# Kernel optimization log

Hardware: AMD Instinct MI355X
Metric: run time of the kernel (lower is better)

The kernel has to match this reference:

```python
import jax, jax.numpy as jnp
import numpy as np

SEQ_LEN = 16384
IN_DIM = 2048
STATE_DIM = 2048


def setup_inputs() -> dict:
    key = jax.random.key(0)
    k_xs, k_lam, k_win, k_c, k_d = jax.random.split(key, 5)
    xs = jax.random.normal(k_xs, (SEQ_LEN, IN_DIM), dtype=jnp.float32)
    # diagonal state-transition values in (0, 1) for stability
    lam = jax.random.uniform(k_lam, (STATE_DIM,), dtype=jnp.float32)
    w_in = jax.random.normal(k_win, (STATE_DIM, IN_DIM), dtype=jnp.float32) / np.float32(np.sqrt(IN_DIM))
    c_out = jax.random.normal(k_c, (IN_DIM, STATE_DIM), dtype=jnp.float32) / np.float32(np.sqrt(STATE_DIM))
    d_skip = jax.random.normal(k_d, (IN_DIM,), dtype=jnp.float32)
    return {"xs": xs, "lam": lam, "w_in": w_in, "c_out": c_out, "d_skip": d_skip}


def _ssm_cell(a, b):
    # Faithful replication of BaseSSMLayer.ssm_cell (including its use of
    # matrix_pow_i * matrix_pow_i for the first component, exactly as in source).
    matrix_pow_i, bx_i = a
    matrix_pow_j, bx_j = b
    return (matrix_pow_i * matrix_pow_i, matrix_pow_j * bx_i + bx_j)


def reference(xs, lam, w_in, c_out, d_skip):
    seq_len = xs.shape[0]
    # discretize: broadcast diagonal lambda over the sequence -> [L, N]
    lambda_elements = jnp.broadcast_to(lam, (seq_len, lam.shape[0]))
    # preprocess_inputs: vmap(w_in @ x) == xs @ w_in.T  -> [L, N]
    w_in_xs = jnp.einsum('li,ni->ln', xs, w_in)
    _, hs = jax.lax.associative_scan(_ssm_cell, (lambda_elements, w_in_xs))
    # postprocess: y_t = C h_t + D * x_t  -> [L, in_dim]
    return jnp.einsum('ln,on->lo', hs, c_out) + xs * d_skip
```

## Files before the change

### kernel.cpp

```cpp
#include <hip/hip_runtime.h>

#define SEQ   16384
#define DIM   2048
#define CHUNK 128
#define NCHUNK (SEQ / CHUNK)

typedef __attribute__((ext_vector_type(8))) short  short8;
typedef __attribute__((ext_vector_type(4))) short  short4v;
typedef __attribute__((ext_vector_type(4))) float  floatx4;

static __device__ __forceinline__ float bf2f(short s) {
    return __uint_as_float(((unsigned)(unsigned short)s) << 16);
}
static __device__ __forceinline__ short f2bf(float f) {
    unsigned u = __float_as_uint(f);
    u += 0x7fff + ((u >> 16) & 1);
    return (short)(u >> 16);
}

#define NB_XS (SEQ * DIM / 4 / 256)
#define NB_W  (DIM * DIM / 4 / 256)
__global__ void cast3_kernel(const float* __restrict__ xs,   short* __restrict__ xs_o,
                             const float* __restrict__ w,    short* __restrict__ w_o,
                             const float* __restrict__ c,    short* __restrict__ c_o)
{
    int b = blockIdx.x;
    const float* in; short* out; int i;
    if (b < NB_XS)            { in = xs; out = xs_o; i = b * 256 + threadIdx.x; }
    else if (b < NB_XS + NB_W){ in = w;  out = w_o;  i = (b - NB_XS) * 256 + threadIdx.x; }
    else                      { in = c;  out = c_o;  i = (b - NB_XS - NB_W) * 256 + threadIdx.x; }
    float4 v = ((const float4*)in)[i];
    short4v s;
    s.x = f2bf(v.x); s.y = f2bf(v.y); s.z = f2bf(v.z); s.w = f2bf(v.w);
    ((short4v*)out)[i] = s;
}


#define BAR   __builtin_amdgcn_s_barrier()
#define PRIO1 __builtin_amdgcn_s_setprio(1)
#define PRIO0 __builtin_amdgcn_s_setprio(0)
#define VMC2  asm volatile("s_waitcnt vmcnt(2)" ::: "memory")
#define VMC1  asm volatile("s_waitcnt vmcnt(1)" ::: "memory")
#define VMC0  asm volatile("s_waitcnt vmcnt(0)" ::: "memory")

#define STAGE_A(b, h, t) do { \
    const short* _s = Abase + (size_t)(h) * 128 * K + (size_t)(t) * 64; \
    __builtin_amdgcn_global_load_lds(_s + gOff0, &As[b][h][c0 * 8], 16, 0, 0); \
    __builtin_amdgcn_global_load_lds(_s + gOff1, &As[b][h][c1 * 8], 16, 0, 0); \
} while (0)
#define STAGE_B(b, h, t) do { \
    const short* _s = Bbase + (size_t)(h) * 128 * K + (size_t)(t) * 64; \
    __builtin_amdgcn_global_load_lds(_s + gOff0, &Bs[b][h][c0 * 8], 16, 0, 0); \
    __builtin_amdgcn_global_load_lds(_s + gOff1, &Bs[b][h][c1 * 8], 16, 0, 0); \
} while (0)

#define READ_A8(dst, b, mh) \
    _Pragma("unroll") \
    for (int mi = 0; mi < 4; mi++) { \
        _Pragma("unroll") \
        for (int ks = 0; ks < 2; ks++) \
            dst[mi][ks] = *(const short8*)&As[b][mh][(arow + mi * 16) * 64 + \
                                                     ((((ks << 2) | quad) ^ sx) << 3)]; \
    }
#define READ_B4(dst, b, nh) \
    _Pragma("unroll") \
    for (int ni = 0; ni < 2; ni++) { \
        _Pragma("unroll") \
        for (int ks = 0; ks < 2; ks++) \
            dst[ni][ks] = *(const short8*)&Bs[b][nh][(brow + ni * 16) * 64 + \
                                                     ((((ks << 2) | quad) ^ sx) << 3)]; \
    }
#define MMA(mh, nh, Aset, Bset) \
    _Pragma("unroll") \
    for (int mi = 0; mi < 4; mi++) { \
        _Pragma("unroll") \
        for (int ni = 0; ni < 2; ni++) { \
            acc[mh][nh][mi][ni] = __builtin_amdgcn_mfma_f32_16x16x32_bf16( \
                Aset[mi][0], Bset[ni][0], acc[mh][nh][mi][ni], 0, 0, 0); \
            acc[mh][nh][mi][ni] = __builtin_amdgcn_mfma_f32_16x16x32_bf16( \
                Aset[mi][1], Bset[ni][1], acc[mh][nh][mi][ni], 0, 0, 0); \
        } \
    }

template<int FUSE>
__global__ __launch_bounds__(512, 2)
void gemm_bt(const short* __restrict__ A, const short* __restrict__ B,
             short* __restrict__ Cbf, float* __restrict__ Cf,
             const float* __restrict__ xs, const float* __restrict__ dskip)
{
    constexpr int K  = DIM;
    constexpr int NT = K / 64;

    __shared__ alignas(16) short As[2][2][128 * 64];
    __shared__ alignas(16) short Bs[2][2][128 * 64];

    const int tid = threadIdx.x;
    const int raw  = blockIdx.y * gridDim.x + blockIdx.x;
    const int xcd  = raw & 7;
    const int slot = raw >> 3;
    const int m0   = ((xcd << 3) | (slot >> 3)) * 256;
    const int n0   = (slot & 7) * 256;

    const int lane = tid & 63;
    const int wv   = tid >> 6;
    const int wrow = wv >> 2;
    const int wcol = wv & 3;
    const int l16  = lane & 15;
    const int quad = lane >> 4;
    const int sx   = l16 & 7;
    const int arow = wrow * 64 + l16;
    const int brow = wcol * 32 + l16;

    const int c0 = tid, c1 = tid + 512;
    const int r0 = c0 >> 3, r1 = c1 >> 3;
    const size_t gOff0 = (size_t)r0 * K + (size_t)((((c0 & 7) ^ (r0 & 7))) * 8);
    const size_t gOff1 = (size_t)r1 * K + (size_t)((((c1 & 7) ^ (r1 & 7))) * 8);
    const short* Abase = A + (size_t)m0 * K;
    const short* Bbase = B + (size_t)n0 * K;

    short8  aE[4][2], aO[4][2], bE[2][2], bO[2][2];
    floatx4 acc[2][2][4][2] = {};

    STAGE_A(0, 0, 0); STAGE_B(0, 0, 0); STAGE_B(0, 1, 0);
    STAGE_A(0, 1, 0);
    VMC1;
    BAR;
    READ_A8(aE, 0, 0); READ_B4(bE, 0, 0);

    for (int i = 0; i < NT / 2; ++i) {
        const int t1 = 2 * i + 1;
        const int t2 = (2 * i + 2) & (NT - 1);

        READ_B4(bO, 0, 1);
        STAGE_A(1, 0, t1); STAGE_B(1, 0, t1);
        PRIO1; MMA(0, 0, aE, bE); PRIO0;
        VMC2;
        BAR;
        READ_A8(aO, 0, 1);
        STAGE_B(1, 1, t1); STAGE_A(1, 1, t1);
        PRIO1; MMA(0, 1, aE, bO); PRIO0;
        VMC2;
        BAR;
        PRIO1; MMA(1, 0, aO, bE); PRIO0;
        READ_B4(bE, 1, 0);
        BAR;
        PRIO1; MMA(1, 1, aO, bO); PRIO0;
        READ_A8(aE, 1, 0);
        VMC1;
        BAR;

        READ_B4(bO, 1, 1);
        STAGE_A(0, 0, t2); STAGE_B(0, 0, t2);
        PRIO1; MMA(0, 0, aE, bE); PRIO0;
        VMC2;
        BAR;

        READ_A8(aO, 1, 1);
        STAGE_B(0, 1, t2); STAGE_A(0, 1, t2);
        PRIO1; MMA(0, 1, aE, bO); PRIO0;
        VMC2;
        BAR;

        PRIO1; MMA(1, 0, aO, bE); PRIO0;
        READ_B4(bE, 0, 0);
        BAR;

        PRIO1; MMA(1, 1, aO, bO); PRIO0;
        READ_A8(aE, 0, 0);
        VMC1;
        BAR;
    }
    VMC0;

    if (FUSE == 0) {
        #pragma unroll
        for (int mh = 0; mh < 2; mh++)
        #pragma unroll
        for (int mi = 0; mi < 4; mi++) {
            const int rb = m0 + wrow * 64 + mh * 128 + mi * 16 + quad * 4;
            #pragma unroll
            for (int nh = 0; nh < 2; nh++)
            #pragma unroll
            for (int ni = 0; ni < 2; ni++) {
                const int cc = n0 + wcol * 32 + nh * 128 + ni * 16 + l16;
                #pragma unroll
                for (int r = 0; r < 4; r++)
                    Cbf[(size_t)(rb + r) * DIM + cc] = f2bf(acc[mh][nh][mi][ni][r]);
            }
        }
    } else {
        float dsk[2][2];
        #pragma unroll
        for (int nh = 0; nh < 2; nh++)
        #pragma unroll
        for (int ni = 0; ni < 2; ni++)
            dsk[nh][ni] = dskip[n0 + wcol * 32 + nh * 128 + ni * 16 + l16];
        #pragma unroll
        for (int mh = 0; mh < 2; mh++)
        #pragma unroll
        for (int mi = 0; mi < 4; mi++) {
            const int rb = m0 + wrow * 64 + mh * 128 + mi * 16 + quad * 4;
            #pragma unroll
            for (int nh = 0; nh < 2; nh++)
            #pragma unroll
            for (int ni = 0; ni < 2; ni++) {
                const int cc = n0 + wcol * 32 + nh * 128 + ni * 16 + l16;
                #pragma unroll
                for (int r = 0; r < 4; r++) {
                    size_t idx = (size_t)(rb + r) * DIM + cc;
                    Cf[idx] = acc[mh][nh][mi][ni][r] + xs[idx] * dsk[nh][ni];
                }
            }
        }
    }
}

__global__ void scan_pass1(const short* __restrict__ bx, const float* __restrict__ lam,
                           float* __restrict__ blockLast)
{
    int q     = blockIdx.x * 256 + threadIdx.x;
    int n     = q * 4;
    int chunk = blockIdx.y;
    float4 lm = *(const float4*)&lam[n];
    const uint2* p = (const uint2*)(bx + (size_t)chunk * CHUNK * DIM) + q;
    float h0 = 0.f, h1 = 0.f, h2 = 0.f, h3 = 0.f;
    #pragma unroll 16
    for (int i = 0; i < CHUNK; i++) {
        uint2 v = p[(size_t)i * (DIM / 4)];
        h0 = fmaf(lm.x, h0, bf2f((short)(v.x & 0xffffu)));
        h1 = fmaf(lm.y, h1, bf2f((short)(v.x >> 16)));
        h2 = fmaf(lm.z, h2, bf2f((short)(v.y & 0xffffu)));
        h3 = fmaf(lm.w, h3, bf2f((short)(v.y >> 16)));
    }
    float4 o; o.x = h0; o.y = h1; o.z = h2; o.w = h3;
    *(float4*)&blockLast[(size_t)chunk * DIM + n] = o;
}

__global__ void scan_pass2(float* __restrict__ blockLast, const float* __restrict__ lam)
{
    int n = blockIdx.x * 256 + threadIdx.x;
    float lm = lam[n];
    float p = lm;
    #pragma unroll
    for (int i = 0; i < 7; i++) p = p * p;
    float carry = 0.f;
    #pragma unroll 4
    for (int c = 0; c < NCHUNK; c++) {
        float t = blockLast[(size_t)c * DIM + n];
        blockLast[(size_t)c * DIM + n] = carry;
        carry = fmaf(p, carry, t);
    }
}

__global__ void scan_pass3(short* __restrict__ bxh, const float* __restrict__ lam,
                           const float* __restrict__ carry)
{
    int q     = blockIdx.x * 256 + threadIdx.x;
    int n     = q * 4;
    int chunk = blockIdx.y;
    float4 lm = *(const float4*)&lam[n];
    float4 cv = *(const float4*)&carry[(size_t)chunk * DIM + n];
    float h0 = cv.x, h1 = cv.y, h2 = cv.z, h3 = cv.w;
    uint2* p = (uint2*)(bxh + (size_t)chunk * CHUNK * DIM) + q;
    #pragma unroll 16
    for (int i = 0; i < CHUNK; i++) {
        uint2 v = p[(size_t)i * (DIM / 4)];
        h0 = fmaf(lm.x, h0, bf2f((short)(v.x & 0xffffu)));
        h1 = fmaf(lm.y, h1, bf2f((short)(v.x >> 16)));
        h2 = fmaf(lm.z, h2, bf2f((short)(v.y & 0xffffu)));
        h3 = fmaf(lm.w, h3, bf2f((short)(v.y >> 16)));
        uint2 o;
        o.x = (unsigned)(unsigned short)f2bf(h0) | ((unsigned)(unsigned short)f2bf(h1) << 16);
        o.y = (unsigned)(unsigned short)f2bf(h2) | ((unsigned)(unsigned short)f2bf(h3) << 16);
        p[(size_t)i * (DIM / 4)] = o;
    }
}

extern "C" void kernel_launch(void* const* d_in, const int* in_sizes, int n_in,
                              void* d_out, int out_size, void* d_ws, size_t ws_size,
                              hipStream_t stream)
{
    const float* xs    = (const float*)d_in[0];
    const float* lam   = (const float*)d_in[1];
    const float* w_in  = (const float*)d_in[2];
    const float* c_out = (const float*)d_in[3];
    const float* dskip = (const float*)d_in[4];
    float* out = (float*)d_out;

    char*  ws    = (char*)d_ws;
    short* bxh   = (short*)ws;
    short* w_bf  = (short*)(ws + (size_t)64 * 1024 * 1024);
    short* c_bf  = (short*)(ws + (size_t)72 * 1024 * 1024);
    short* xs_bf = (short*)d_out;
    float* blkl  = (float*)((char*)d_out + (size_t)100 * 1024 * 1024);

    cast3_kernel<<<NB_XS + 2 * NB_W, 256, 0, stream>>>(xs, xs_bf, w_in, w_bf, c_out, c_bf);

    dim3 ggrid(DIM / 256, SEQ / 256);
    gemm_bt<0><<<ggrid, 512, 0, stream>>>(xs_bf, w_bf, bxh, nullptr, nullptr, nullptr);

    dim3 sgrid(DIM / 1024, NCHUNK);
    scan_pass1<<<sgrid, 256, 0, stream>>>(bxh, lam, blkl);
    scan_pass2<<<DIM / 256, 256, 0, stream>>>(blkl, lam);
    scan_pass3<<<sgrid, 256, 0, stream>>>(bxh, lam, blkl);

    gemm_bt<1><<<ggrid, 512, 0, stream>>>(bxh, c_bf, nullptr, out, xs, dskip);
}
```

Measured before the change: 569.1 us.

## Fuse chunk-local scan reduction into GEMM epilogue and deepen load pipeline

The first GEMM's epilogue now computes each 128-row chunk's decayed sum of the fp32 accumulators. It weights rows by powers of lambda, reduces across lanes and waves through LDS, and writes the per-chunk carry, which removes the separate scan_pass1 kernel and its re-read of the bf16 intermediate. The GEMM main loop is also rescheduled to prefetch two K-tiles ahead, with finer vmcnt waits and the loop no longer unrolled. Chunk sums now come from fp32 rather than rounded bf16 values, which changes numerics slightly. The extra epilogue work adds register pressure and cost to the GEMM.

Result: no change. 562.8 us (-1.1%).

```diff
diff --git a/kernel.cpp b/kernel.cpp
--- a/kernel.cpp
+++ b/kernel.cpp
@@ -39,8 +39,10 @@
 #define BAR   __builtin_amdgcn_s_barrier()
 #define PRIO1 __builtin_amdgcn_s_setprio(1)
 #define PRIO0 __builtin_amdgcn_s_setprio(0)
-#define VMC2  asm volatile("s_waitcnt vmcnt(2)" ::: "memory")
-#define VMC1  asm volatile("s_waitcnt vmcnt(1)" ::: "memory")
+#define VMC12 asm volatile("s_waitcnt vmcnt(12)" ::: "memory")
+#define VMC10 asm volatile("s_waitcnt vmcnt(10)" ::: "memory")
+#define VMC8  asm volatile("s_waitcnt vmcnt(8)" ::: "memory")
+#define VMC6  asm volatile("s_waitcnt vmcnt(6)" ::: "memory")
 #define VMC0  asm volatile("s_waitcnt vmcnt(0)" ::: "memory")
 
 #define STAGE_A(b, h, t) do { \
@@ -86,7 +88,8 @@
 __global__ __launch_bounds__(512, 2)
 void gemm_bt(const short* __restrict__ A, const short* __restrict__ B,
              short* __restrict__ Cbf, float* __restrict__ Cf,
-             const float* __restrict__ xs, const float* __restrict__ dskip)
+             const float* __restrict__ xs, const float* __restrict__ dskip,
+             const float* __restrict__ lamv, float* __restrict__ blkl)
 {
     constexpr int K  = DIM;
     constexpr int NT = K / 64;
@@ -118,57 +121,46 @@
     const short* Abase = A + (size_t)m0 * K;
     const short* Bbase = B + (size_t)n0 * K;
 
-    short8  aE[4][2], aO[4][2], bE[2][2], bO[2][2];
+    short8  A0v[4][2], A1v[4][2], B0v[2][2], B1v[2][2];
     floatx4 acc[2][2][4][2] = {};
 
-    STAGE_A(0, 0, 0); STAGE_B(0, 0, 0); STAGE_B(0, 1, 0);
-    STAGE_A(0, 1, 0);
-    VMC1;
+    STAGE_A(0, 0, 0); STAGE_A(0, 1, 0); STAGE_B(0, 0, 0); STAGE_B(0, 1, 0);
+    STAGE_B(1, 0, 1); STAGE_A(1, 0, 1); STAGE_A(1, 1, 1); STAGE_B(1, 1, 1);
+    VMC8;
     BAR;
-    READ_A8(aE, 0, 0); READ_B4(bE, 0, 0);
-
+    READ_B4(B0v, 0, 0);
+    READ_A8(A0v, 0, 0);
+
+    #pragma unroll 1
     for (int i = 0; i < NT / 2; ++i) {
-        const int t1 = 2 * i + 1;
-        const int t2 = (2 * i + 2) & (NT - 1);
-
-        READ_B4(bO, 0, 1);
-        STAGE_A(1, 0, t1); STAGE_B(1, 0, t1);
-        PRIO1; MMA(0, 0, aE, bE); PRIO0;
-        VMC2;
-        BAR;
-        READ_A8(aO, 0, 1);
-        STAGE_B(1, 1, t1); STAGE_A(1, 1, t1);
-        PRIO1; MMA(0, 1, aE, bO); PRIO0;
-        VMC2;
-        BAR;
-        PRIO1; MMA(1, 0, aO, bE); PRIO0;
-        READ_B4(bE, 1, 0);
-        BAR;
-        PRIO1; MMA(1, 1, aO, bO); PRIO0;
-        READ_A8(aE, 1, 0);
-        VMC1;
-        BAR;
-
-        READ_B4(bO, 1, 1);
-        STAGE_A(0, 0, t2); STAGE_B(0, 0, t2);
-        PRIO1; MMA(0, 0, aE, bE); PRIO0;
-        VMC2;
-        BAR;
-
-        READ_A8(aO, 1, 1);
-        STAGE_B(0, 1, t2); STAGE_A(0, 1, t2);
-        PRIO1; MMA(0, 1, aE, bO); PRIO0;
-        VMC2;
-        BAR;
-
-        PRIO1; MMA(1, 0, aO, bE); PRIO0;
-        READ_B4(bE, 0, 0);
-        BAR;
-
-        PRIO1; MMA(1, 1, aO, bO); PRIO0;
-        READ_A8(aE, 0, 0);
-        VMC1;
-        BAR;
+        const bool more = (i < NT / 2 - 1);
+        const int tE = 2 * i + 2;
+        const int tO = 2 * i + 3;
+
+        VMC10; READ_A8(A1v, 0, 1);
+        PRIO1; MMA(0, 0, A0v, B0v); PRIO0; BAR;
+        VMC8;  READ_B4(B1v, 0, 1);
+        PRIO1; MMA(1, 0, A1v, B0v); PRIO0; BAR;
+        VMC6;  READ_B4(B0v, 1, 0);
+        if (more) { STAGE_B(0, 0, tE); STAGE_A(0, 0, tE); STAGE_A(0, 1, tE); STAGE_B(0, 1, tE); }
+        PRIO1; MMA(0, 1, A0v, B1v); PRIO0; BAR;
+        VMC12; READ_A8(A0v, 1, 0);
+        PRIO1; MMA(1, 1, A1v, B1v); PRIO0; BAR;
+
+        VMC10; READ_A8(A1v, 1, 1);
+        PRIO1; MMA(0, 0, A0v, B0v); PRIO0; BAR;
+
+        VMC8;  READ_B4(B1v, 1, 1);
+        PRIO1; MMA(1, 0, A1v, B0v); PRIO0; BAR;
+
+        VMC6;
+        if (more) { READ_B4(B0v, 0, 0); }
+        if (more) { STAGE_B(1, 0, tO); STAGE_A(1, 0, tO); STAGE_A(1, 1, tO); STAGE_B(1, 1, tO); }
+        PRIO1; MMA(0, 1, A0v, B1v); PRIO0; BAR;
+
+        VMC12;
+        if (more) { READ_A8(A0v, 0, 0); }
+        PRIO1; MMA(1, 1, A1v, B1v); PRIO0; BAR;
     }
     VMC0;
 
@@ -187,6 +179,54 @@
                 for (int r = 0; r < 4; r++)
                     Cbf[(size_t)(rb + r) * DIM + cc] = f2bf(acc[mh][nh][mi][ni][r]);
             }
+        }
+        float Pacc[2][2][2];
+        #pragma unroll
+        for (int nh = 0; nh < 2; nh++)
+        #pragma unroll
+        for (int ni = 0; ni < 2; ni++) {
+            const int cc = n0 + wcol * 32 + nh * 128 + ni * 16 + l16;
+            const float l = lamv[cc];
+            const float l2 = l * l, l4 = l2 * l2, l8 = l4 * l4;
+            const float l16p = l8 * l8, l32 = l16p * l16p, l64 = l32 * l32;
+            const int k3 = 19 - 16 * wrow - quad;
+            float q = 1.f;
+            q = (k3 & 1)  ? q * l4   : q;
+            q = (k3 & 2)  ? q * l8   : q;
+            q = (k3 & 4)  ? q * l16p : q;
+            q = (k3 & 8)  ? q * l32  : q;
+            q = (k3 & 16) ? q * l64  : q;
+            #pragma unroll
+            for (int mh = 0; mh < 2; mh++) {
+                float s = 0.f, qq = q;
+                #pragma unroll
+                for (int mi = 3; mi >= 0; --mi) {
+                    floatx4 a = acc[mh][nh][mi][ni];
+                    float inner = fmaf(fmaf(fmaf(a[0], l, a[1]), l, a[2]), l, a[3]);
+                    s = fmaf(qq, inner, s);
+                    qq *= l16p;
+                }
+                Pacc[mh][nh][ni] = s;
+            }
+        }
+        float* Pl = (float*)&As[0][0][0];
+        #pragma unroll
+        for (int mh = 0; mh < 2; mh++)
+        #pragma unroll
+        for (int nh = 0; nh < 2; nh++)
+        #pragma unroll
+        for (int ni = 0; ni < 2; ni++) {
+            float v = Pacc[mh][nh][ni];
+            v += __shfl_xor(v, 16);
+            v += __shfl_xor(v, 32);
+            if (lane < 16)
+                Pl[wrow * 512 + mh * 256 + (wcol * 32 + nh * 128 + ni * 16 + l16)] = v;
+        }
+        __syncthreads();
+        {
+            const int mh = tid >> 8, cl = tid & 255;
+            float v = Pl[mh * 256 + cl] + Pl[512 + mh * 256 + cl];
+            blkl[(size_t)((m0 >> 7) + mh) * DIM + (n0 + cl)] = v;
         }
     } else {
         float dsk[2][2];
@@ -213,27 +253,6 @@
             }
         }
     }
-}
-
-__global__ void scan_pass1(const short* __restrict__ bx, const float* __restrict__ lam,
-                           float* __restrict__ blockLast)
-{
-    int q     = blockIdx.x * 256 + threadIdx.x;
-    int n     = q * 4;
-    int chunk = blockIdx.y;
-    float4 lm = *(const float4*)&lam[n];
-    const uint2* p = (const uint2*)(bx + (size_t)chunk * CHUNK * DIM) + q;
-    float h0 = 0.f, h1 = 0.f, h2 = 0.f, h3 = 0.f;
-    #pragma unroll 16
-    for (int i = 0; i < CHUNK; i++) {
-        uint2 v = p[(size_t)i * (DIM / 4)];
-        h0 = fmaf(lm.x, h0, bf2f((short)(v.x & 0xffffu)));
-        h1 = fmaf(lm.y, h1, bf2f((short)(v.x >> 16)));
-        h2 = fmaf(lm.z, h2, bf2f((short)(v.y & 0xffffu)));
-        h3 = fmaf(lm.w, h3, bf2f((short)(v.y >> 16)));
-    }
-    float4 o; o.x = h0; o.y = h1; o.z = h2; o.w = h3;
-    *(float4*)&blockLast[(size_t)chunk * DIM + n] = o;
 }
 
 __global__ void scan_pass2(float* __restrict__ blockLast, const float* __restrict__ lam)
@@ -297,12 +316,13 @@
     cast3_kernel<<<NB_XS + 2 * NB_W, 256, 0, stream>>>(xs, xs_bf, w_in, w_bf, c_out, c_bf);
 
     dim3 ggrid(DIM / 256, SEQ / 256);
-    gemm_bt<0><<<ggrid, 512, 0, stream>>>(xs_bf, w_bf, bxh, nullptr, nullptr, nullptr);
-
+    gemm_bt<0><<<ggrid, 512, 0, stream>>>(xs_bf, w_bf, bxh, nullptr, nullptr, nullptr,
+                                          lam, blkl);
+
+    scan_pass2<<<DIM / 256, 256, 0, stream>>>(blkl, lam);
     dim3 sgrid(DIM / 1024, NCHUNK);
-    scan_pass1<<<sgrid, 256, 0, stream>>>(bxh, lam, blkl);
-    scan_pass2<<<DIM / 256, 256, 0, stream>>>(blkl, lam);
     scan_pass3<<<sgrid, 256, 0, stream>>>(bxh, lam, blkl);
 
-    gemm_bt<1><<<ggrid, 512, 0, stream>>>(bxh, c_bf, nullptr, out, xs, dskip);
-}
+    gemm_bt<1><<<ggrid, 512, 0, stream>>>(bxh, c_bf, nullptr, out, xs, dskip,
+                                          nullptr, nullptr);
+}
```

## Fuse chunk-local scan reduction into GEMM epilogue and merge carry passes

Applied to the files above, without the earlier changes.

The first GEMM's epilogue now computes, from its fp32 accumulators, each 128-row chunk's decayed sum using powers of lambda, reduces it across waves through shared memory and writes the per-chunk partials. This removes scan_pass1's full re-read of the bf16 projection. scan_pass2 is folded into the final scan kernel: each chunk block recomputes its incoming carry serially over all preceding chunk partials, which costs quadratic redundant reads of the small partial buffer. The partials come from unrounded fp32 values instead of bf16, so numerics shift slightly.

Result: faster. 547.7 us (-3.8%).

```diff
diff --git a/kernel.cpp b/kernel.cpp
--- a/kernel.cpp
+++ b/kernel.cpp
@@ -86,7 +86,8 @@
 __global__ __launch_bounds__(512, 2)
 void gemm_bt(const short* __restrict__ A, const short* __restrict__ B,
              short* __restrict__ Cbf, float* __restrict__ Cf,
-             const float* __restrict__ xs, const float* __restrict__ dskip)
+             const float* __restrict__ xs, const float* __restrict__ dskip,
+             const float* __restrict__ lamv, float* __restrict__ blkl)
 {
     constexpr int K  = DIM;
     constexpr int NT = K / 64;
@@ -188,6 +189,54 @@
                     Cbf[(size_t)(rb + r) * DIM + cc] = f2bf(acc[mh][nh][mi][ni][r]);
             }
         }
+        float Pacc[2][2][2];
+        #pragma unroll
+        for (int nh = 0; nh < 2; nh++)
+        #pragma unroll
+        for (int ni = 0; ni < 2; ni++) {
+            const int cc = n0 + wcol * 32 + nh * 128 + ni * 16 + l16;
+            const float l = lamv[cc];
+            const float l2 = l * l, l4 = l2 * l2, l8 = l4 * l4;
+            const float l16p = l8 * l8, l32 = l16p * l16p, l64 = l32 * l32;
+            const int k3 = 19 - 16 * wrow - quad;
+            float q = 1.f;
+            q = (k3 & 1)  ? q * l4   : q;
+            q = (k3 & 2)  ? q * l8   : q;
+            q = (k3 & 4)  ? q * l16p : q;
+            q = (k3 & 8)  ? q * l32  : q;
+            q = (k3 & 16) ? q * l64  : q;
+            #pragma unroll
+            for (int mh = 0; mh < 2; mh++) {
+                float s = 0.f, qq = q;
+                #pragma unroll
+                for (int mi = 3; mi >= 0; --mi) {
+                    floatx4 a = acc[mh][nh][mi][ni];
+                    float inner = fmaf(fmaf(fmaf(a[0], l, a[1]), l, a[2]), l, a[3]);
+                    s = fmaf(qq, inner, s);
+                    qq *= l16p;
+                }
+                Pacc[mh][nh][ni] = s;
+            }
+        }
+        float* Pl = (float*)&As[0][0][0];
+        #pragma unroll
+        for (int mh = 0; mh < 2; mh++)
+        #pragma unroll
+        for (int nh = 0; nh < 2; nh++)
+        #pragma unroll
+        for (int ni = 0; ni < 2; ni++) {
+            float v = Pacc[mh][nh][ni];
+            v += __shfl_xor(v, 16);
+            v += __shfl_xor(v, 32);
+            if (lane < 16)
+                Pl[wrow * 512 + mh * 256 + (wcol * 32 + nh * 128 + ni * 16 + l16)] = v;
+        }
+        __syncthreads();
+        {
+            const int mh = tid >> 8, cl = tid & 255;
+            float v = Pl[mh * 256 + cl] + Pl[512 + mh * 256 + cl];
+            blkl[(size_t)((m0 >> 7) + mh) * DIM + (n0 + cl)] = v;
+        }
     } else {
         float dsk[2][2];
         #pragma unroll
@@ -215,52 +264,25 @@
     }
 }
 
-__global__ void scan_pass1(const short* __restrict__ bx, const float* __restrict__ lam,
-                           float* __restrict__ blockLast)
+__global__ void scan_pass23(short* __restrict__ bxh, const float* __restrict__ lam,
+                            const float* __restrict__ blkl)
 {
     int q     = blockIdx.x * 256 + threadIdx.x;
     int n     = q * 4;
     int chunk = blockIdx.y;
     float4 lm = *(const float4*)&lam[n];
-    const uint2* p = (const uint2*)(bx + (size_t)chunk * CHUNK * DIM) + q;
+    float p0 = lm.x, p1 = lm.y, p2 = lm.z, p3 = lm.w;
+    #pragma unroll
+    for (int i = 0; i < 7; i++) { p0 *= p0; p1 *= p1; p2 *= p2; p3 *= p3; }
     float h0 = 0.f, h1 = 0.f, h2 = 0.f, h3 = 0.f;
-    #pragma unroll 16
-    for (int i = 0; i < CHUNK; i++) {
-        uint2 v = p[(size_t)i * (DIM / 4)];
-        h0 = fmaf(lm.x, h0, bf2f((short)(v.x & 0xffffu)));
-        h1 = fmaf(lm.y, h1, bf2f((short)(v.x >> 16)));
-        h2 = fmaf(lm.z, h2, bf2f((short)(v.y & 0xffffu)));
-        h3 = fmaf(lm.w, h3, bf2f((short)(v.y >> 16)));
-    }
-    float4 o; o.x = h0; o.y = h1; o.z = h2; o.w = h3;
-    *(float4*)&blockLast[(size_t)chunk * DIM + n] = o;
-}
-
-__global__ void scan_pass2(float* __restrict__ blockLast, const float* __restrict__ lam)
-{
-    int n = blockIdx.x * 256 + threadIdx.x;
-    float lm = lam[n];
-    float p = lm;
-    #pragma unroll
-    for (int i = 0; i < 7; i++) p = p * p;
-    float carry = 0.f;
     #pragma unroll 4
-    for (int c = 0; c < NCHUNK; c++) {
-        float t = blockLast[(size_t)c * DIM + n];
-        blockLast[(size_t)c * DIM + n] = carry;
-        carry = fmaf(p, carry, t);
-    }
-}
-
-__global__ void scan_pass3(short* __restrict__ bxh, const float* __restrict__ lam,
-                           const float* __restrict__ carry)
-{
-    int q     = blockIdx.x * 256 + threadIdx.x;
-    int n     = q * 4;
-    int chunk = blockIdx.y;
-    float4 lm = *(const float4*)&lam[n];
-    float4 cv = *(const float4*)&carry[(size_t)chunk * DIM + n];
-    float h0 = cv.x, h1 = cv.y, h2 = cv.z, h3 = cv.w;
+    for (int j = 0; j < chunk; ++j) {
+        float4 s = *(const float4*)&blkl[(size_t)j * DIM + n];
+        h0 = fmaf(p0, h0, s.x);
+        h1 = fmaf(p1, h1, s.y);
+        h2 = fmaf(p2, h2, s.z);
+        h3 = fmaf(p3, h3, s.w);
+    }
     uint2* p = (uint2*)(bxh + (size_t)chunk * CHUNK * DIM) + q;
     #pragma unroll 16
     for (int i = 0; i < CHUNK; i++) {
@@ -297,12 +319,12 @@
     cast3_kernel<<<NB_XS + 2 * NB_W, 256, 0, stream>>>(xs, xs_bf, w_in, w_bf, c_out, c_bf);
 
     dim3 ggrid(DIM / 256, SEQ / 256);
-    gemm_bt<0><<<ggrid, 512, 0, stream>>>(xs_bf, w_bf, bxh, nullptr, nullptr, nullptr);
+    gemm_bt<0><<<ggrid, 512, 0, stream>>>(xs_bf, w_bf, bxh, nullptr, nullptr, nullptr,
+                                          lam, blkl);
 
     dim3 sgrid(DIM / 1024, NCHUNK);
-    scan_pass1<<<sgrid, 256, 0, stream>>>(bxh, lam, blkl);
-    scan_pass2<<<DIM / 256, 256, 0, stream>>>(blkl, lam);
-    scan_pass3<<<sgrid, 256, 0, stream>>>(bxh, lam, blkl);
-
-    gemm_bt<1><<<ggrid, 512, 0, stream>>>(bxh, c_bf, nullptr, out, xs, dskip);
-}
+    scan_pass23<<<sgrid, 256, 0, stream>>>(bxh, lam, blkl);
+
+    gemm_bt<1><<<ggrid, 512, 0, stream>>>(bxh, c_bf, nullptr, out, xs, dskip,
+                                          nullptr, nullptr);
+}
```
